# Kernel optimization log

Measured on AMD Instinct MI355X. Metric: run time of the kernel, lower is better.

Reference implementation:

```python
import jax, jax.numpy as jnp
import numpy as np

B, IN_UNITS, IN_CHANNELS, NUM_UNITS, UNIT_SIZE = 256, 8, 1152, 10, 16
NUM_ITERS = 3


def setup_inputs() -> dict:
    key = jax.random.key(0)
    k1, k2 = jax.random.split(key)
    x = jax.random.normal(k1, (B, IN_UNITS, IN_CHANNELS), dtype=jnp.float32)
    # W from nn.Parameter(torch.randn(1, in_channels, num_units, unit_size, in_units)); drop leading 1
    W = jax.random.normal(k2, (IN_CHANNELS, NUM_UNITS, UNIT_SIZE, IN_UNITS), dtype=jnp.float32)
    return {"x": x, "W": W}


def reference(x, W):
    # x: [B, in_units=i, in_channels=j]; original transposes to [B, j, i]
    # u_hat = W @ x : [B, j, n, u]
    batch = x.shape[0]
    u_hat = jnp.einsum('jnui,bij->bjnu', W, x)
    b = jnp.zeros((IN_CHANNELS, NUM_UNITS), dtype=x.dtype)  # b_ij [j, n]
    v = None
    for _ in range(NUM_ITERS):
        # legacy F.softmax on 4D [1,j,n,1] -> dim=1 = in_channels axis
        c = jax.nn.softmax(b, axis=0)  # [j, n]
        s = jnp.einsum('jn,bjnu->bnu', c, u_hat)  # s_j: [B, n, u]
        # squash over dim=2 of [B,1,n,u,1] == num_units axis (axis=1 here)
        mag_sq = jnp.sum(s * s, axis=1, keepdims=True)  # [B, 1, u]
        v = (mag_sq / (1.0 + mag_sq)) * (s / jnp.sqrt(mag_sq))  # [B, n, u]
        # agreement: mean over batch of <u_hat, v>
        b = b + jnp.einsum('bjnu,bnu->jn', u_hat, v) / batch
    return v[..., None]  # [B, num_units, unit_size, 1] == v_j.squeeze(1)
```

## Files before the change

kernel.cpp:

```cpp
#include <hip/hip_runtime.h>
#include <stdint.h>

#define B   256
#define IU  8
#define JC  1152
#define NN  10
#define UU  16
#define NU  160
#define JN  11520
#define WROW 1280
#define NP  9216
#define KB  72

typedef short bf16x8 __attribute__((ext_vector_type(8)));
typedef float f32x4  __attribute__((ext_vector_type(4)));

__device__ __forceinline__ short f2bf(float f) {
    union { float f; uint32_t u; } cv; cv.f = f;
    uint32_t u = cv.u;
    uint32_t r = u + 0x7fffu + ((u >> 16) & 1u);
    return (short)(r >> 16);
}
__device__ __forceinline__ float bf2f(short h) {
    union { uint32_t u; float f; } cv; cv.u = ((uint32_t)(unsigned short)h) << 16;
    return cv.f;
}
__device__ __forceinline__ uint32_t bfbits(float f) {
    union { float f; uint32_t u; } cv; cv.f = f;
    return (cv.u + 0x7fffu + ((cv.u >> 16) & 1u)) >> 16;
}
__device__ __forceinline__ uint32_t pk2(float a, float b) {
    return bfbits(a) | (bfbits(b) << 16);
}

__global__ void __launch_bounds__(256, 2)
k_gemm1(const float* __restrict__ xg, const float* __restrict__ wg,
        const float* __restrict__ eblog, const float* __restrict__ expsum,
        float* __restrict__ s_part) {
    const int kb = blockIdx.x, mt = blockIdx.y;
    const int tid = threadIdx.x;
    const int wv = tid >> 6, lane = tid & 63;
    const int q = lane >> 4, l16 = lane & 15;
    const int b0 = mt * 32;
    const int jb0 = kb * 16;
    const int mfrag = wv >> 1;
    const int ntb = (wv & 1) * 5;

    __shared__ __align__(16) short As[8 * 32 * 8];
    __shared__ __align__(16) short Bs[8 * 160 * 8];
    __shared__ float inv_s[NN];

    if (eblog && tid < NN) inv_s[tid] = 1.f / expsum[tid];

    f32x4 acc[5];
    #pragma unroll
    for (int nt = 0; nt < 5; ++nt) acc[nt] = (f32x4){0.f, 0.f, 0.f, 0.f};

    for (int jc = 0; jc < 2; ++jc) {
        const int j0 = jb0 + jc * 8;
        __syncthreads();
        #pragma unroll
        for (int p = 0; p < 2; ++p) {
            int idx = tid + 256 * p;
            int jq  = idx & 1;
            int row = idx >> 1;
            int bl = row >> 3, ii = row & 7;
            const float4 xv = *reinterpret_cast<const float4*>(
                &xg[(size_t)(b0 + bl) * NP + ii * JC + j0 + jq*4]);
            int jjb = jq * 4;
            As[((jjb+0)*32 + bl)*8 + ii] = f2bf(xv.x);
            As[((jjb+1)*32 + bl)*8 + ii] = f2bf(xv.y);
            As[((jjb+2)*32 + bl)*8 + ii] = f2bf(xv.z);
            As[((jjb+3)*32 + bl)*8 + ii] = f2bf(xv.w);
        }
        #pragma unroll
        for (int p = 0; p < 5; ++p) {
            int ridx = tid + 256 * p;
            int jj = ridx / 160;
            int nu = ridx - jj * 160;
            int j  = j0 + jj;
            const float4* wp = reinterpret_cast<const float4*>(
                &wg[(size_t)j * WROW + (size_t)nu * 8]);
            float4 f0 = wp[0], f1 = wp[1];
            int nn = nu >> 4;
            float cc = eblog ? eblog[j * NN + nn] * inv_s[nn]
                             : (1.0f / (float)JC);
            uint4 d;
            d.x = pk2(f0.x * cc, f0.y * cc);
            d.y = pk2(f0.z * cc, f0.w * cc);
            d.z = pk2(f1.x * cc, f1.y * cc);
            d.w = pk2(f1.z * cc, f1.w * cc);
            *reinterpret_cast<uint4*>(&Bs[(size_t)ridx * 8]) = d;
        }
        __syncthreads();
        #pragma unroll
        for (int s = 0; s < 2; ++s) {
            int jj = s*4 + q;
            bf16x8 av = *reinterpret_cast<const bf16x8*>(
                &As[((jj*32 + mfrag*16 + l16) << 3)]);
            #pragma unroll
            for (int nt = 0; nt < 5; ++nt) {
                bf16x8 bv = *reinterpret_cast<const bf16x8*>(
                    &Bs[((jj*160 + (ntb + nt)*16 + l16) << 3)]);
                acc[nt] = __builtin_amdgcn_mfma_f32_16x16x32_bf16(av, bv, acc[nt], 0, 0, 0);
            }
        }
    }
    float* dst = s_part + (size_t)(kb*8 + mt) * 5120;
    #pragma unroll
    for (int nt = 0; nt < 5; ++nt)
        #pragma unroll
        for (int reg = 0; reg < 4; ++reg)
            dst[(mfrag*16 + q*4 + reg) * 160 + (ntb + nt)*16 + l16] = acc[nt][reg];
}

__global__ void __launch_bounds__(320, 2)
k_reduce_s(const float* __restrict__ s_part, float* __restrict__ vdst) {
    const int b = blockIdx.x, tid = threadIdx.x;
    const int t = tid % 160, kq = tid / 160;
    const int mt = b >> 5, bl = b & 31;
    const size_t off = (size_t)mt * 5120 + bl * 160 + t;

    float s = 0.f;
    for (int r = 0; r < 36; ++r)
        s += s_part[(size_t)(kq*36 + r) * 40960 + off];

    __shared__ float red[2][160];
    __shared__ float sv[NU];
    __shared__ float fb[UU];
    red[kq][t] = s;
    __syncthreads();
    if (tid < NU) sv[tid] = red[0][tid] + red[1][tid];
    __syncthreads();
    if (tid < UU) {
        float m = 0.f;
        #pragma unroll
        for (int n = 0; n < NN; ++n) { float z = sv[n*16 + tid]; m = fmaf(z, z, m); }
        fb[tid] = sqrtf(m) / (1.f + m);
    }
    __syncthreads();
    if (tid < NU)
        vdst[(size_t)b * NU + tid] = sv[tid] * fb[tid & 15];
}

__global__ void __launch_bounds__(256, 2)
k_vxg(const float* __restrict__ vg, const float* __restrict__ xg,
      float* __restrict__ G, float* __restrict__ expsum) {
    const int np0 = blockIdx.x * 64, m0 = blockIdx.y * 32;
    const int tid = threadIdx.x;
    const int wv = tid >> 6, lane = tid & 63;
    const int q = lane >> 4, l16 = lane & 15;

    if (blockIdx.x == 0 && blockIdx.y == 0 && tid < NN) expsum[tid] = 0.f;

    __shared__ __align__(16) short Ash[8 * 32 * 8];
    __shared__ __align__(16) short Asl[8 * 32 * 8];
    __shared__ __align__(16) short Bsh[8 * 64 * 8];
    __shared__ __align__(16) short Bsl[8 * 64 * 8];

    f32x4 acc[2];
    acc[0] = (f32x4){0.f,0.f,0.f,0.f};
    acc[1] = (f32x4){0.f,0.f,0.f,0.f};

    for (int ks = 0; ks < 4; ++ks) {
        const int b0 = ks * 64;
        __syncthreads();
        #pragma unroll
        for (int p = 0; p < 8; ++p) {
            int idx = tid + 256 * p;
            int bb = idx >> 5, ml = idx & 31;
            float vv = vg[(size_t)(b0 + bb) * NU + m0 + ml];
            short hi = f2bf(vv);
            short lo = f2bf(vv - bf2f(hi));
            int a = ((bb >> 3) * 32 + ml) * 8 + (bb & 7);
            Ash[a] = hi; Asl[a] = lo;
        }
        #pragma unroll
        for (int p = 0; p < 16; ++p) {
            int idx = tid + 256 * p;
            int bb = idx >> 6, nl = idx & 63;
            float xv = xg[(size_t)(b0 + bb) * NP + np0 + nl];
            short hi = f2bf(xv);
            short lo = f2bf(xv - bf2f(hi));
            int a = ((bb >> 3) * 64 + nl) * 8 + (bb & 7);
            Bsh[a] = hi; Bsl[a] = lo;
        }
        __syncthreads();
        #pragma unroll
        for (int s = 0; s < 2; ++s) {
            int kc = s*4 + q;
            bf16x8 bh = *reinterpret_cast<const bf16x8*>(&Bsh[((kc*64 + wv*16 + l16) << 3)]);
            bf16x8 bl = *reinterpret_cast<const bf16x8*>(&Bsl[((kc*64 + wv*16 + l16) << 3)]);
            #pragma unroll
            for (int mtl = 0; mtl < 2; ++mtl) {
                bf16x8 ah = *reinterpret_cast<const bf16x8*>(&Ash[((kc*32 + mtl*16 + l16) << 3)]);
                bf16x8 al = *reinterpret_cast<const bf16x8*>(&Asl[((kc*32 + mtl*16 + l16) << 3)]);
                acc[mtl] = __builtin_amdgcn_mfma_f32_16x16x32_bf16(ah, bh, acc[mtl], 0, 0, 0);
                acc[mtl] = __builtin_amdgcn_mfma_f32_16x16x32_bf16(ah, bl, acc[mtl], 0, 0, 0);
                acc[mtl] = __builtin_amdgcn_mfma_f32_16x16x32_bf16(al, bh, acc[mtl], 0, 0, 0);
            }
        }
    }
    #pragma unroll
    for (int mtl = 0; mtl < 2; ++mtl)
        #pragma unroll
        for (int reg = 0; reg < 4; ++reg) {
            int m  = m0 + mtl*16 + q*4 + reg;
            G[(size_t)m * NP + np0 + wv*16 + l16] = acc[mtl][reg];
        }
}

__global__ void k_wg_db(const float* __restrict__ wg, const float* __restrict__ G,
                        float* __restrict__ blog, float* __restrict__ eblog,
                        float* __restrict__ expsum, int t0) {
    const int j0 = blockIdx.x * 64, n = blockIdx.y;
    const int tid = threadIdx.x;
    const int jl = tid & 63, up = tid >> 6;
    const int j = j0 + jl;

    const float4* wp = reinterpret_cast<const float4*>(
        wg + (size_t)j * WROW + n * 128 + up * 32);
    float acc = 0.f;
    #pragma unroll
    for (int q4 = 0; q4 < 4; ++q4) {
        int u = up*4 + q4;
        const float* gp = G + (size_t)(n*16 + u) * NP + j;
        float4 w0 = wp[q4*2], w1 = wp[q4*2 + 1];
        acc = fmaf(w0.x, gp[0*JC], acc);
        acc = fmaf(w0.y, gp[1*JC], acc);
        acc = fmaf(w0.z, gp[2*JC], acc);
        acc = fmaf(w0.w, gp[3*JC], acc);
        acc = fmaf(w1.x, gp[4*JC], acc);
        acc = fmaf(w1.y, gp[5*JC], acc);
        acc = fmaf(w1.z, gp[6*JC], acc);
        acc = fmaf(w1.w, gp[7*JC], acc);
    }
    __shared__ float red[4][64];
    red[up][jl] = acc;
    __syncthreads();
    if (tid < 64) {
        int jj = j0 + tid;
        float d = (red[0][tid] + red[1][tid] + red[2][tid] + red[3][tid])
                  * (1.f / (float)B);
        float nb = t0 ? d : (blog[jj*NN + n] + d);
        blog[jj*NN + n] = nb;
        float e = __expf(nb);
        eblog[jj*NN + n] = e;
        float s = e;
        s += __shfl_xor(s, 1);  s += __shfl_xor(s, 2);
        s += __shfl_xor(s, 4);  s += __shfl_xor(s, 8);
        s += __shfl_xor(s, 16); s += __shfl_xor(s, 32);
        if (tid == 0) atomicAdd(&expsum[n], s);
    }
}

extern "C" void kernel_launch(void* const* d_in, const int* in_sizes, int n_in,
                              void* d_out, int out_size, void* d_ws, size_t ws_size,
                              hipStream_t stream) {
    const float* x = (const float*)d_in[0];
    const float* w = (const float*)d_in[1];
    float* out = (float*)d_out;

    float* ws     = (float*)d_ws;
    float* blog   = ws;
    float* eblog  = blog + JN;
    float* expsum = eblog + JN;
    float* v      = expsum + 16;
    float* s_part = v + (size_t)B*NU;
    float* G      = s_part + (size_t)KB * 40960;

    for (int t = 0; t < 3; ++t) {
        k_gemm1<<<dim3(KB, 8), 256, 0, stream>>>(
            x, w, (t == 0) ? nullptr : eblog, expsum, s_part);
        k_reduce_s<<<B, 320, 0, stream>>>(s_part, (t == 2) ? out : v);
        if (t < 2) {
            k_vxg<<<dim3(144, 5), 256, 0, stream>>>(v, x, G, expsum);
            k_wg_db<<<dim3(18, 10), 256, 0, stream>>>(w, G, blog, eblog, expsum,
                                                      (t == 0) ? 1 : 0);
        }
    }
}
```

Before: 147.2 us.

## Precompute bf16 x/W once and feed GEMM via direct global-to-LDS loads

Adds a one-time prep kernel that converts x into a transposed bf16 layout and W into bf16. The per-iteration GEMM then streams these with global_load_lds instead of reloading fp32 and converting each pass. The softmax-weighted W is now written as bf16 by the routing-logit kernel, using unnormalized exp weights, and the 1/sum normalization moves into the reduction kernel. Each GEMM block covers twice as many input channels, halving the partial sums, and G reuses the s_part buffer. The cost is the extra prep pass and bf16 rounding of W times an unnormalized exponential.

```diff
diff --git a/kernel.cpp b/kernel.cpp
--- a/kernel.cpp
+++ b/kernel.cpp
@@ -10,7 +10,7 @@
 #define JN  11520
 #define WROW 1280
 #define NP  9216
-#define KB  72
+#define KB  36
 
 typedef short bf16x8 __attribute__((ext_vector_type(8)));
 typedef float f32x4  __attribute__((ext_vector_type(4)));
@@ -32,105 +32,126 @@
 __device__ __forceinline__ uint32_t pk2(float a, float b) {
     return bfbits(a) | (bfbits(b) << 16);
 }
+__device__ __forceinline__ void gload16(const void* g, void* l) {
+    __builtin_amdgcn_global_load_lds(
+        (const __attribute__((address_space(1))) void*)g,
+        (__attribute__((address_space(3))) void*)l, 16, 0, 0);
+}
+
+__global__ void __launch_bounds__(256)
+k_prep(const float* __restrict__ xg, const float* __restrict__ wg,
+       short* __restrict__ wbf, short* __restrict__ xbf) {
+    const int bid = blockIdx.x, tid = threadIdx.x;
+    if (bid < 576) {
+        const int jt = bid % 18, rt = bid / 18;
+        const int j0 = jt * 64, r0 = rt * 64;
+        __shared__ short T[64][72];
+        #pragma unroll
+        for (int p = 0; p < 4; ++p) {
+            int idx = tid + 256 * p;
+            int row = idx >> 4;
+            int c4  = (idx & 15) * 4;
+            float4 xv = *reinterpret_cast<const float4*>(
+                &xg[(size_t)(r0 + row) * JC + j0 + c4]);
+            T[c4+0][row] = f2bf(xv.x);
+            T[c4+1][row] = f2bf(xv.y);
+            T[c4+2][row] = f2bf(xv.z);
+            T[c4+3][row] = f2bf(xv.w);
+        }
+        __syncthreads();
+        #pragma unroll
+        for (int p = 0; p < 2; ++p) {
+            int idx = tid + 256 * p;
+            int jl = idx >> 3;
+            int r8 = (idx & 7) * 8;
+            uint4 d = *reinterpret_cast<const uint4*>(&T[jl][r8]);
+            *reinterpret_cast<uint4*>(&xbf[(size_t)(j0 + jl) * 2048 + r0 + r8]) = d;
+        }
+    } else {
+        const int b2 = bid - 576;
+        size_t base = (size_t)b2 * 2048 + (size_t)tid * 8;
+        float4 f0 = *reinterpret_cast<const float4*>(&wg[base]);
+        float4 f1 = *reinterpret_cast<const float4*>(&wg[base + 4]);
+        uint4 d;
+        d.x = pk2(f0.x, f0.y); d.y = pk2(f0.z, f0.w);
+        d.z = pk2(f1.x, f1.y); d.w = pk2(f1.z, f1.w);
+        *reinterpret_cast<uint4*>(&wbf[base]) = d;
+    }
+}
 
 __global__ void __launch_bounds__(256, 2)
-k_gemm1(const float* __restrict__ xg, const float* __restrict__ wg,
-        const float* __restrict__ eblog, const float* __restrict__ expsum,
+k_gemm1(const short* __restrict__ xbf, const short* __restrict__ wbf,
         float* __restrict__ s_part) {
     const int kb = blockIdx.x, mt = blockIdx.y;
     const int tid = threadIdx.x;
     const int wv = tid >> 6, lane = tid & 63;
     const int q = lane >> 4, l16 = lane & 15;
     const int b0 = mt * 32;
-    const int jb0 = kb * 16;
+    const int jb0 = kb * 32;
     const int mfrag = wv >> 1;
     const int ntb = (wv & 1) * 5;
 
     __shared__ __align__(16) short As[8 * 32 * 8];
     __shared__ __align__(16) short Bs[8 * 160 * 8];
-    __shared__ float inv_s[NN];
-
-    if (eblog && tid < NN) inv_s[tid] = 1.f / expsum[tid];
 
     f32x4 acc[5];
     #pragma unroll
     for (int nt = 0; nt < 5; ++nt) acc[nt] = (f32x4){0.f, 0.f, 0.f, 0.f};
 
-    for (int jc = 0; jc < 2; ++jc) {
+    for (int jc = 0; jc < 4; ++jc) {
         const int j0 = jb0 + jc * 8;
         __syncthreads();
-        #pragma unroll
-        for (int p = 0; p < 2; ++p) {
-            int idx = tid + 256 * p;
-            int jq  = idx & 1;
-            int row = idx >> 1;
-            int bl = row >> 3, ii = row & 7;
-            const float4 xv = *reinterpret_cast<const float4*>(
-                &xg[(size_t)(b0 + bl) * NP + ii * JC + j0 + jq*4]);
-            int jjb = jq * 4;
-            As[((jjb+0)*32 + bl)*8 + ii] = f2bf(xv.x);
-            As[((jjb+1)*32 + bl)*8 + ii] = f2bf(xv.y);
-            As[((jjb+2)*32 + bl)*8 + ii] = f2bf(xv.z);
-            As[((jjb+3)*32 + bl)*8 + ii] = f2bf(xv.w);
-        }
+        gload16(xbf + ((size_t)(j0 + (tid >> 5)) * 2048 + (size_t)(b0 + (tid & 31)) * 8),
+                &As[tid * 8]);
+        const short* wsrc = wbf + (size_t)j0 * WROW;
         #pragma unroll
         for (int p = 0; p < 5; ++p) {
             int ridx = tid + 256 * p;
-            int jj = ridx / 160;
-            int nu = ridx - jj * 160;
-            int j  = j0 + jj;
-            const float4* wp = reinterpret_cast<const float4*>(
-                &wg[(size_t)j * WROW + (size_t)nu * 8]);
-            float4 f0 = wp[0], f1 = wp[1];
-            int nn = nu >> 4;
-            float cc = eblog ? eblog[j * NN + nn] * inv_s[nn]
-                             : (1.0f / (float)JC);
-            uint4 d;
-            d.x = pk2(f0.x * cc, f0.y * cc);
-            d.y = pk2(f0.z * cc, f0.w * cc);
-            d.z = pk2(f1.x * cc, f1.y * cc);
-            d.w = pk2(f1.z * cc, f1.w * cc);
-            *reinterpret_cast<uint4*>(&Bs[(size_t)ridx * 8]) = d;
+            gload16(wsrc + (size_t)ridx * 8, &Bs[ridx * 8]);
         }
         __syncthreads();
         #pragma unroll
         for (int s = 0; s < 2; ++s) {
-            int jj = s*4 + q;
+            int jj = s * 4 + q;
             bf16x8 av = *reinterpret_cast<const bf16x8*>(
-                &As[((jj*32 + mfrag*16 + l16) << 3)]);
+                &As[(jj * 32 + mfrag * 16 + l16) << 3]);
             #pragma unroll
             for (int nt = 0; nt < 5; ++nt) {
                 bf16x8 bv = *reinterpret_cast<const bf16x8*>(
-                    &Bs[((jj*160 + (ntb + nt)*16 + l16) << 3)]);
+                    &Bs[(jj * 160 + (ntb + nt) * 16 + l16) << 3]);
                 acc[nt] = __builtin_amdgcn_mfma_f32_16x16x32_bf16(av, bv, acc[nt], 0, 0, 0);
             }
         }
     }
-    float* dst = s_part + (size_t)(kb*8 + mt) * 5120;
+    float* dst = s_part + (size_t)(kb * 8 + mt) * 5120;
     #pragma unroll
     for (int nt = 0; nt < 5; ++nt)
         #pragma unroll
         for (int reg = 0; reg < 4; ++reg)
-            dst[(mfrag*16 + q*4 + reg) * 160 + (ntb + nt)*16 + l16] = acc[nt][reg];
+            dst[(mfrag * 16 + q * 4 + reg) * 160 + (ntb + nt) * 16 + l16] = acc[nt][reg];
 }
 
 __global__ void __launch_bounds__(320, 2)
-k_reduce_s(const float* __restrict__ s_part, float* __restrict__ vdst) {
+k_reduce_s(const float* __restrict__ s_part, float* __restrict__ vdst,
+           const float* __restrict__ expsum, int t0) {
     const int b = blockIdx.x, tid = threadIdx.x;
     const int t = tid % 160, kq = tid / 160;
     const int mt = b >> 5, bl = b & 31;
     const size_t off = (size_t)mt * 5120 + bl * 160 + t;
 
+    __shared__ float invn[NN];
+    if (tid < NN) invn[tid] = t0 ? (1.f / (float)JC) : 1.f / expsum[tid];
+
     float s = 0.f;
-    for (int r = 0; r < 36; ++r)
-        s += s_part[(size_t)(kq*36 + r) * 40960 + off];
+    for (int r = 0; r < 18; ++r)
+        s += s_part[(size_t)(kq * 18 + r) * 40960 + off];
 
     __shared__ float red[2][160];
     __shared__ float sv[NU];
     __shared__ float fb[UU];
     red[kq][t] = s;
     __syncthreads();
-    if (tid < NU) sv[tid] = red[0][tid] + red[1][tid];
+    if (tid < NU) sv[tid] = (red[0][tid] + red[1][tid]) * invn[tid >> 4];
     __syncthreads();
     if (tid < UU) {
         float m = 0.f;
@@ -211,7 +232,7 @@
 }
 
 __global__ void k_wg_db(const float* __restrict__ wg, const float* __restrict__ G,
-                        float* __restrict__ blog, float* __restrict__ eblog,
+                        float* __restrict__ blog, short* __restrict__ wbf,
                         float* __restrict__ expsum, int t0) {
     const int j0 = blockIdx.x * 64, n = blockIdx.y;
     const int tid = threadIdx.x;
@@ -220,12 +241,16 @@
 
     const float4* wp = reinterpret_cast<const float4*>(
         wg + (size_t)j * WROW + n * 128 + up * 32);
+    float4 w[8];
+    #pragma unroll
+    for (int k = 0; k < 8; ++k) w[k] = wp[k];
+
     float acc = 0.f;
     #pragma unroll
     for (int q4 = 0; q4 < 4; ++q4) {
         int u = up*4 + q4;
         const float* gp = G + (size_t)(n*16 + u) * NP + j;
-        float4 w0 = wp[q4*2], w1 = wp[q4*2 + 1];
+        float4 w0 = w[q4*2], w1 = w[q4*2 + 1];
         acc = fmaf(w0.x, gp[0*JC], acc);
         acc = fmaf(w0.y, gp[1*JC], acc);
         acc = fmaf(w0.z, gp[2*JC], acc);
@@ -236,6 +261,8 @@
         acc = fmaf(w1.w, gp[7*JC], acc);
     }
     __shared__ float red[4][64];
+    __shared__ float esh[64];
+    __shared__ __align__(16) short Wsh[64][136];
     red[up][jl] = acc;
     __syncthreads();
     if (tid < 64) {
@@ -245,12 +272,32 @@
         float nb = t0 ? d : (blog[jj*NN + n] + d);
         blog[jj*NN + n] = nb;
         float e = __expf(nb);
-        eblog[jj*NN + n] = e;
+        esh[tid] = e;
         float s = e;
         s += __shfl_xor(s, 1);  s += __shfl_xor(s, 2);
         s += __shfl_xor(s, 4);  s += __shfl_xor(s, 8);
         s += __shfl_xor(s, 16); s += __shfl_xor(s, 32);
         if (tid == 0) atomicAdd(&expsum[n], s);
+    }
+    __syncthreads();
+    const float e = esh[jl];
+    #pragma unroll
+    for (int q4 = 0; q4 < 4; ++q4) {
+        float4 a = w[q4*2], bq = w[q4*2 + 1];
+        uint4 d;
+        d.x = pk2(a.x * e, a.y * e);
+        d.y = pk2(a.z * e, a.w * e);
+        d.z = pk2(bq.x * e, bq.y * e);
+        d.w = pk2(bq.z * e, bq.w * e);
+        *reinterpret_cast<uint4*>(&Wsh[jl][up*32 + q4*8]) = d;
+    }
+    __syncthreads();
+    #pragma unroll
+    for (int p = 0; p < 4; ++p) {
+        int idx = tid + 256 * p;
+        int jj = idx >> 4, seg = idx & 15;
+        uint4 d = *reinterpret_cast<const uint4*>(&Wsh[jj][seg * 8]);
+        *reinterpret_cast<uint4*>(&wbf[(size_t)(j0 + jj) * WROW + n*128 + seg*8]) = d;
     }
 }
 
@@ -263,19 +310,21 @@
 
     float* ws     = (float*)d_ws;
     float* blog   = ws;
-    float* eblog  = blog + JN;
-    float* expsum = eblog + JN;
+    float* expsum = blog + JN;
     float* v      = expsum + 16;
-    float* s_part = v + (size_t)B*NU;
-    float* G      = s_part + (size_t)KB * 40960;
-
+    short* wbf    = (short*)(v + (size_t)B * NU);
+    short* xbf    = wbf + (size_t)JC * WROW;
+    float* s_part = (float*)(xbf + (size_t)JC * 2048);
+    float* G      = s_part;
+
+    k_prep<<<1296, 256, 0, stream>>>(x, w, wbf, xbf);
     for (int t = 0; t < 3; ++t) {
-        k_gemm1<<<dim3(KB, 8), 256, 0, stream>>>(
-            x, w, (t == 0) ? nullptr : eblog, expsum, s_part);
-        k_reduce_s<<<B, 320, 0, stream>>>(s_part, (t == 2) ? out : v);
+        k_gemm1<<<dim3(KB, 8), 256, 0, stream>>>(xbf, wbf, s_part);
+        k_reduce_s<<<B, 320, 0, stream>>>(s_part, (t == 2) ? out : v, expsum,
+                                          (t == 0) ? 1 : 0);
         if (t < 2) {
             k_vxg<<<dim3(144, 5), 256, 0, stream>>>(v, x, G, expsum);
-            k_wg_db<<<dim3(18, 10), 256, 0, stream>>>(w, G, blog, eblog, expsum,
+            k_wg_db<<<dim3(18, 10), 256, 0, stream>>>(w, G, blog, wbf, expsum,
                                                       (t == 0) ? 1 : 0);
         }
     }
```

Measured after the change: 144.1 us. 2.1% less time.
